# Performance work log

Hardware: AMD Instinct MI355X
Metric: run time of the kernel (lower is better)

Reference implementation:

```python
import jax, jax.numpy as jnp
import numpy as np

HEADS = 8
K = 3            # kernel_size per axis
RPB = 2 * K - 1  # rel-pos-bias extent per axis
EPS = 1e-5


def _nbr(dim, k):
    # NATTEN-style clamped window: shift window to stay fully inside [0, dim)
    q = jnp.arange(dim)
    start = jnp.clip(q - k // 2, 0, dim - k)
    nbr = start[:, None] + jnp.arange(k)[None, :]       # (dim, k) neighbor coords
    rel = nbr - q[:, None] + (k - 1)                    # (dim, k) in [0, 2k-2]
    return nbr, rel


def _instance_norm(x):
    # InstanceNorm3d, affine=False: normalize over spatial dims per (B, C)
    m = jnp.mean(x, axis=(2, 3, 4), keepdims=True)
    v = jnp.var(x, axis=(2, 3, 4), keepdims=True)
    return (x - m) * jax.lax.rsqrt(v + EPS)


def setup_inputs() -> dict:
    key = jax.random.key(0)
    ks = jax.random.split(key, 10)
    B, C, H, W, Z = 1, 128, 32, 32, 32
    Cf = 4 * C
    s = 0.02
    return {
        "x": jax.random.normal(ks[0], (B, C, H, W, Z), jnp.float32),
        "w_qkv": jax.random.normal(ks[1], (3 * C, C), jnp.float32) * s,
        "b_qkv": jnp.zeros((3 * C,), jnp.float32),
        "rpb": jax.random.normal(ks[2], (HEADS, RPB, RPB, RPB), jnp.float32) * s,
        "w_proj": jax.random.normal(ks[3], (C, C), jnp.float32) * s,
        "b_proj": jnp.zeros((C,), jnp.float32),
        "w_ffn1": jax.random.normal(ks[4], (Cf, C), jnp.float32) * s,
        "b_ffn1": jnp.zeros((Cf,), jnp.float32),
        "w_ffn2": jax.random.normal(ks[5], (C, Cf), jnp.float32) * s,
        "b_ffn2": jnp.zeros((C,), jnp.float32),
    }


def reference(x, w_qkv, b_qkv, rpb, w_proj, b_proj, w_ffn1, b_ffn1, w_ffn2, b_ffn2):
    B, C, H, W, Z = x.shape
    hd = C // HEADS
    N = H * W * Z
    KK = K ** 3

    # ---- SAM: 3D neighborhood self-attention ----
    xt = x.reshape(B, C, N).transpose(0, 2, 1)                 # (B, N, C)
    qkv = xt @ w_qkv.T + b_qkv                                  # (B, N, 3C)
    q, k_, v = jnp.split(qkv, 3, axis=-1)
    split = lambda t: t.reshape(B, N, HEADS, hd).transpose(0, 2, 1, 3)  # (B, h, N, d)
    q, k_, v = split(q), split(k_), split(v)

    nh, rh = _nbr(H, K)
    nw, rw = _nbr(W, K)
    nz, rz = _nbr(Z, K)
    # flat neighbor token index per (h, w, z, kh, kw, kz)
    nbr = ((nh[:, None, None, :, None, None] * W
            + nw[None, :, None, None, :, None]) * Z
           + nz[None, None, :, None, None, :]).reshape(N, KK)   # (N, 27)
    # flat rel-pos-bias index
    bidx = ((rh[:, None, None, :, None, None] * RPB
             + rw[None, :, None, None, :, None]) * RPB
            + rz[None, None, :, None, None, :]).reshape(N, KK)  # (N, 27)

    kg = k_[:, :, nbr]                                          # (B, h, N, 27, d)
    vg = v[:, :, nbr]                                           # (B, h, N, 27, d)
    bias = rpb.reshape(HEADS, RPB ** 3)[:, bidx]                # (h, N, 27)

    scale = jnp.asarray(hd, x.dtype) ** -0.5
    attn = jnp.einsum('bhnd,bhnkd->bhnk', q * scale, kg) + bias
    attn = jax.nn.softmax(attn, axis=-1)
    out = jnp.einsum('bhnk,bhnkd->bhnd', attn, vg)              # (B, h, N, d)
    out = out.transpose(0, 2, 1, 3).reshape(B, N, C) @ w_proj.T + b_proj
    x5 = out.transpose(0, 2, 1).reshape(B, C, H, W, Z)

    # ---- norm_in ----
    x5 = _instance_norm(x5)

    # ---- FFN (mmcv-style, GELU, residual identity) ----
    t = x5.reshape(B, C, N).transpose(0, 2, 1)                  # (B, N, C)
    t = t + (jax.nn.gelu(t @ w_ffn1.T + b_ffn1) @ w_ffn2.T + b_ffn2)
    x5 = t.transpose(0, 2, 1).reshape(B, C, H, W, Z)

    # ---- norm_out ----
    return _instance_norm(x5)
```

## Files before the change

### kernel.cpp

```cpp
#include <hip/hip_runtime.h>
#include <hip/hip_bf16.h>
#include <math.h>

#define NPOS 32768
#define CCH  128
#define C3   384
#define CF   512
#define NSH  16

typedef __attribute__((ext_vector_type(8))) short short8;
typedef __attribute__((ext_vector_type(4))) float f32x4;

__device__ inline float bf2f(unsigned short u) {
    union { unsigned int i; float f; } x; x.i = ((unsigned int)u) << 16; return x.f;
}
__device__ inline unsigned short f2bf(float f) {
    union { float f; unsigned int i; } x; x.f = f;
    unsigned int r = x.i + 0x7FFFu + ((x.i >> 16) & 1u);
    return (unsigned short)(r >> 16);
}
__device__ inline float lo_bf(unsigned int u) {
    union { unsigned int i; float f; } x; x.i = u << 16; return x.f;
}
__device__ inline float hi_bf(unsigned int u) {
    union { unsigned int i; float f; } x; x.i = u & 0xffff0000u; return x.f;
}

__global__ __launch_bounds__(256) void qkv_gemm_kernel(
    const unsigned short* __restrict__ A,
    const unsigned short* __restrict__ B,
    const float* __restrict__ bias,
    unsigned short* __restrict__ outh)
{
    __shared__ alignas(16) unsigned short As[128 * 40];
    __shared__ alignas(16) unsigned short Bs[128 * 40];

    const int tid  = threadIdx.x;
    const int lane = tid & 63;
    const int wave = tid >> 6;
    const int wm = wave & 1, wn = wave >> 1;
    const int row0 = blockIdx.y * 128;
    const int col0 = blockIdx.x * 128;

    const f32x4 fzero = {0.f, 0.f, 0.f, 0.f};
    f32x4 acc[4][4];
    #pragma unroll
    for (int i = 0; i < 4; ++i)
        #pragma unroll
        for (int j = 0; j < 4; ++j) acc[i][j] = fzero;

    const int lr = lane & 15;
    const int lk = (lane >> 4) * 8;

    for (int kt = 0; kt < CCH; kt += 32) {
        #pragma unroll
        for (int it = 0; it < 2; ++it) {
            const int c = tid + it * 256;
            const int r = c >> 2;
            const int p = (c & 3) * 8;
            *(uint4*)&As[r * 40 + p] = *(const uint4*)&A[(size_t)(row0 + r) * CCH + kt + p];
            *(uint4*)&Bs[r * 40 + p] = *(const uint4*)&B[(size_t)(col0 + r) * CCH + kt + p];
        }
        __syncthreads();
        short8 af[4], bfr[4];
        #pragma unroll
        for (int i = 0; i < 4; ++i)
            af[i]  = *(const short8*)&As[(wm * 64 + i * 16 + lr) * 40 + lk];
        #pragma unroll
        for (int j = 0; j < 4; ++j)
            bfr[j] = *(const short8*)&Bs[(wn * 64 + j * 16 + lr) * 40 + lk];
        #pragma unroll
        for (int i = 0; i < 4; ++i)
            #pragma unroll
            for (int j = 0; j < 4; ++j)
                acc[i][j] = __builtin_amdgcn_mfma_f32_16x16x32_bf16(
                                af[i], bfr[j], acc[i][j], 0, 0, 0);
        __syncthreads();
    }

    const int gr0 = row0 + wm * 64 + (lane >> 4) * 4;
    const int gc0 = col0 + wn * 64 + lr;
    #pragma unroll
    for (int j = 0; j < 4; ++j) {
        const int gc  = gc0 + j * 16;
        const int sel = gc >> 4;
        const int ch  = gc & 15;
        const float bv = bias[gc];
        #pragma unroll
        for (int i = 0; i < 4; ++i) {
            #pragma unroll
            for (int r = 0; r < 4; ++r) {
                const int gr = gr0 + i * 16 + r;
                outh[((size_t)sel * NPOS + gr) * 16 + ch] = f2bf(acc[i][j][r] + bv);
            }
        }
    }
}

__global__ __launch_bounds__(256) void attn_tiled(
    const unsigned short* __restrict__ qkv,
    const float* __restrict__ rpb,
    unsigned short* __restrict__ out)
{
    __shared__ unsigned int ksu[288 * 8];
    __shared__ unsigned int vsu[288 * 8];
    __shared__ unsigned int qsu[32 * 8];
    __shared__ float logits[32 * 29];
    __shared__ float rpbs[125];
    __shared__ float sinv[32];

    const int t  = threadIdx.x;
    const int line = ((blockIdx.x & 7) << 7) + (blockIdx.x >> 3);
    const int h  = blockIdx.y;
    const int w0 = line & 31, h0 = line >> 5;
    const int n0 = (h0 << 10) + (w0 << 5);
    const int sh0 = min(max(h0 - 1, 0), 29);
    const int sw0 = min(max(w0 - 1, 0), 29);
    const int rh_off = sh0 - h0 + 2;
    const int rw_off = sw0 - w0 + 2;

    if (t < 64) {
        const int pos = t >> 1, part = t & 1;
        const uint4 raw = *(const uint4*)&qkv[((size_t)h * NPOS + n0 + pos) * 16 + part * 8];
        *(uint4*)&qsu[pos * 8 + part * 4] = raw;
    } else if (t < 192) {
        const int i = t - 64;
        if (i < 125) rpbs[i] = rpb[h * 125 + i];
    }
    for (int c = t; c < 1152; c += 256) {
        const int p = c >> 2, part = c & 3;
        const int ihw = p >> 5, z = p & 31;
        const int ih = (ihw * 11) >> 5;
        const int iw = ihw - 3 * ih;
        const int n = ((sh0 + ih) << 10) + ((sw0 + iw) << 5) + z;
        const int kv = part >> 1;
        const uint4 raw = *(const uint4*)&qkv[((size_t)(8 + kv * 8 + h) * NPOS + n) * 16
                                              + (part & 1) * 8];
        unsigned int* d = ((kv == 0) ? ksu : vsu) + p * 8 + (part & 1) * 4;
        *(uint4*)d = raw;
    }
    __syncthreads();

    {
        const int q = t >> 3, j = t & 7;
        const int sz = min(max(q - 1, 0), 29);
        const int rz_off = sz - q + 2;
        float qf[16];
        #pragma unroll
        for (int d2 = 0; d2 < 8; ++d2) {
            const unsigned int u = qsu[q * 8 + d2];
            qf[2 * d2] = lo_bf(u); qf[2 * d2 + 1] = hi_bf(u);
        }
        float lv[4];
        int nkk = 0;
        for (int kk = j; kk < 27; kk += 8) {
            const int ihw = kk / 3, dz = kk - 3 * ihw;
            const int ih = ihw / 3,  iw = ihw - 3 * ih;
            const int p = ihw * 32 + sz + dz;
            float a = 0.f;
            #pragma unroll
            for (int d2 = 0; d2 < 8; ++d2) {
                const unsigned int u = ksu[p * 8 + d2];
                a += qf[2 * d2] * lo_bf(u) + qf[2 * d2 + 1] * hi_bf(u);
            }
            const int bidx = ((ih + rh_off) * 5 + (iw + rw_off)) * 5 + (dz + rz_off);
            lv[nkk++] = a * 0.25f + rpbs[bidx];
        }
        float mx = -1e30f;
        #pragma unroll
        for (int u = 0; u < 4; ++u) if (u < nkk) mx = fmaxf(mx, lv[u]);
        mx = fmaxf(mx, __shfl_xor(mx, 1));
        mx = fmaxf(mx, __shfl_xor(mx, 2));
        mx = fmaxf(mx, __shfl_xor(mx, 4));
        float s = 0.f;
        int u = 0;
        for (int kk = j; kk < 27; kk += 8) {
            const float e = __expf(lv[u++] - mx);
            logits[q * 29 + kk] = e;
            s += e;
        }
        s += __shfl_xor(s, 1);
        s += __shfl_xor(s, 2);
        s += __shfl_xor(s, 4);
        if (j == 0) sinv[q] = 1.f / s;
    }
    __syncthreads();

    {
        const int q = t >> 3, d2 = t & 7;
        const int sz = min(max(q - 1, 0), 29);
        float ax = 0.f, ay = 0.f;
        #pragma unroll
        for (int kk = 0; kk < 27; ++kk) {
            const int p = (kk / 3) * 32 + sz + (kk % 3);
            const float w = logits[q * 29 + kk];
            const unsigned int u = vsu[p * 8 + d2];
            ax += w * lo_bf(u); ay += w * hi_bf(u);
        }
        const float inv = sinv[q];
        const unsigned int o = ((unsigned int)f2bf(ay * inv) << 16)
                             |  (unsigned int)f2bf(ax * inv);
        *(unsigned int*)&out[(size_t)(n0 + q) * CCH + h * 16 + d2 * 2] = o;
    }
}

__global__ __launch_bounds__(256) void proj_stats_kernel(
    const unsigned short* __restrict__ attnO,
    const unsigned short* __restrict__ wproj,
    const float* __restrict__ b_proj,
    unsigned short* __restrict__ x5b,
    float* __restrict__ stats)
{
    __shared__ float red[256];

    const int t    = threadIdx.x;
    const int lane = t & 63;
    const int wn   = t >> 6;
    const int lr = lane & 15;
    const int lg = lane >> 4;
    const int lk = lg * 8;
    const int n0 = blockIdx.x * 64;
    const int sh = (blockIdx.x & (NSH - 1)) * 256;

    red[t] = 0.f;

    short8 wf[2][4];
    #pragma unroll
    for (int j = 0; j < 2; ++j)
        #pragma unroll
        for (int ks = 0; ks < 4; ++ks)
            wf[j][ks] = *(const short8*)&wproj[(wn * 32 + j * 16 + lr) * CCH + ks * 32 + lk];

    const f32x4 fzero = {0.f, 0.f, 0.f, 0.f};
    f32x4 acc[4][2];
    #pragma unroll
    for (int i = 0; i < 4; ++i)
        #pragma unroll
        for (int j = 0; j < 2; ++j) acc[i][j] = fzero;

    #pragma unroll
    for (int ks = 0; ks < 4; ++ks) {
        short8 af[4];
        #pragma unroll
        for (int i = 0; i < 4; ++i)
            af[i] = *(const short8*)&attnO[(size_t)(n0 + i * 16 + lr) * CCH + ks * 32 + lk];
        #pragma unroll
        for (int i = 0; i < 4; ++i)
            #pragma unroll
            for (int j = 0; j < 2; ++j)
                acc[i][j] = __builtin_amdgcn_mfma_f32_16x16x32_bf16(
                                af[i], wf[j][ks], acc[i][j], 0, 0, 0);
    }
    __syncthreads();

    #pragma unroll
    for (int j = 0; j < 2; ++j) {
        const int gc = wn * 32 + j * 16 + lr;
        const float bv = b_proj[gc];
        float s = 0.f, q = 0.f;
        #pragma unroll
        for (int i = 0; i < 4; ++i)
            #pragma unroll
            for (int r = 0; r < 4; ++r) {
                const int gr = i * 16 + lg * 4 + r;
                const float v = acc[i][j][r] + bv;
                s += v; q += v * v;
                x5b[(size_t)(n0 + gr) * CCH + gc] = f2bf(v);
            }
        atomicAdd(&red[gc], s);
        atomicAdd(&red[128 + gc], q);
    }
    __syncthreads();
    if (t < 128) {
        atomicAdd(&stats[sh + t],       red[t]);
        atomicAdd(&stats[sh + 128 + t], red[128 + t]);
    }
}

__global__ __launch_bounds__(256) void ffn_fused_kernel(
    const unsigned short* __restrict__ x5b,
    const unsigned short* __restrict__ w1,
    const float* __restrict__ b1,
    const unsigned short* __restrict__ w2,
    const float* __restrict__ b2,
    float* __restrict__ stats,
    unsigned short* __restrict__ tTb)
{
    __shared__ alignas(16) unsigned short pool[2 * 8704];
    unsigned short* As = pool;
    unsigned short* Hs = pool + 8704;
    __shared__ float red[256];
    __shared__ float ms[128];
    __shared__ float rss[128];

    const int t    = threadIdx.x;
    const int lane = t & 63;
    const int wn   = t >> 6;
    const int lr = lane & 15;
    const int lg = lane >> 4;
    const int lk = lg * 8;
    const int n0 = blockIdx.x * 64;
    const int sh = (blockIdx.x & (NSH - 1)) * 256;
    const float invN = 1.f / (float)NPOS;
    const f32x4 fzero = {0.f, 0.f, 0.f, 0.f};

    red[t] = 0.f;
    if (t < 128) {
        float s0 = 0.f, s1 = 0.f;
        #pragma unroll
        for (int s = 0; s < NSH; ++s) {
            s0 += stats[s * 256 + t];
            s1 += stats[s * 256 + 128 + t];
        }
        const float m = s0 * invN;
        const float v = s1 * invN - m * m;
        ms[t]  = m;
        rss[t] = rsqrtf(v + 1e-5f);
    }
    uint4 px[4];
    #pragma unroll
    for (int it = 0; it < 4; ++it) {
        const int idx = t + it * 256;
        const int row = idx >> 4, c0 = (idx & 15) * 8;
        px[it] = *(const uint4*)&x5b[(size_t)(n0 + row) * CCH + c0];
    }
    __syncthreads();

    #pragma unroll
    for (int it = 0; it < 4; ++it) {
        const int idx = t + it * 256;
        const int row = idx >> 4, c0 = (idx & 15) * 8;
        unsigned int u[4] = {px[it].x, px[it].y, px[it].z, px[it].w};
        #pragma unroll
        for (int p = 0; p < 4; ++p) {
            const int c = c0 + 2 * p;
            const float a = (lo_bf(u[p]) - ms[c])     * rss[c];
            const float b = (hi_bf(u[p]) - ms[c + 1]) * rss[c + 1];
            u[p] = ((unsigned int)f2bf(b) << 16) | (unsigned int)f2bf(a);
        }
        uint4 w; w.x = u[0]; w.y = u[1]; w.z = u[2]; w.w = u[3];
        *(uint4*)&As[row * 136 + c0] = w;
    }
    __syncthreads();

    f32x4 acc[4][2];
    #pragma unroll
    for (int i = 0; i < 4; ++i)
        #pragma unroll
        for (int j = 0; j < 2; ++j) acc[i][j] = fzero;

    #pragma unroll 1
    for (int cc = 0; cc < 4; ++cc) {
        short8 w1f[2][4];
        #pragma unroll
        for (int j = 0; j < 2; ++j)
            #pragma unroll
            for (int ks = 0; ks < 4; ++ks)
                w1f[j][ks] = *(const short8*)&w1[
                    (size_t)(cc * 128 + wn * 32 + j * 16 + lr) * CCH + ks * 32 + lk];

        f32x4 hacc[4][2];
        #pragma unroll
        for (int i = 0; i < 4; ++i)
            #pragma unroll
            for (int j = 0; j < 2; ++j) hacc[i][j] = fzero;
        #pragma unroll
        for (int ks = 0; ks < 4; ++ks) {
            short8 af[4];
            #pragma unroll
            for (int i = 0; i < 4; ++i)
                af[i] = *(const short8*)&As[(i * 16 + lr) * 136 + ks * 32 + lk];
            #pragma unroll
            for (int i = 0; i < 4; ++i)
                #pragma unroll
                for (int j = 0; j < 2; ++j)
                    hacc[i][j] = __builtin_amdgcn_mfma_f32_16x16x32_bf16(
                                    af[i], w1f[j][ks], hacc[i][j], 0, 0, 0);
        }

        short8 w2f[2][4];
        #pragma unroll
        for (int j = 0; j < 2; ++j)
            #pragma unroll
            for (int ks = 0; ks < 4; ++ks)
                w2f[j][ks] = *(const short8*)&w2[
                    (size_t)(wn * 32 + j * 16 + lr) * CF + cc * 128 + ks * 32 + lk];

        #pragma unroll
        for (int j = 0; j < 2; ++j) {
            const int gc = wn * 32 + j * 16 + lr;
            const float bv = b1[cc * 128 + gc];
            #pragma unroll
            for (int i = 0; i < 4; ++i)
                #pragma unroll
                for (int r = 0; r < 4; ++r) {
                    float v = hacc[i][j][r] + bv;
                    const float g = 0.7978845608028654f * (v + 0.044715f * v * v * v);
                    const float e = __expf(2.f * g);
                    v = v * (e / (e + 1.f));
                    Hs[(i * 16 + lg * 4 + r) * 136 + gc] = f2bf(v);
                }
        }
        __syncthreads();

        #pragma unroll
        for (int ks = 0; ks < 4; ++ks) {
            short8 af[4];
            #pragma unroll
            for (int i = 0; i < 4; ++i)
                af[i] = *(const short8*)&Hs[(i * 16 + lr) * 136 + ks * 32 + lk];
            #pragma unroll
            for (int i = 0; i < 4; ++i)
                #pragma unroll
                for (int j = 0; j < 2; ++j)
                    acc[i][j] = __builtin_amdgcn_mfma_f32_16x16x32_bf16(
                                    af[i], w2f[j][ks], acc[i][j], 0, 0, 0);
        }
        __syncthreads();
    }

    #pragma unroll
    for (int j = 0; j < 2; ++j) {
        const int gc = wn * 32 + j * 16 + lr;
        const float bv = b2[gc];
        float s = 0.f, q = 0.f;
        #pragma unroll
        for (int i = 0; i < 4; ++i)
            #pragma unroll
            for (int r = 0; r < 4; ++r) {
                const int gr = i * 16 + lg * 4 + r;
                const float v = acc[i][j][r] + bv + bf2f(As[gr * 136 + gc]);
                acc[i][j][r] = v;
                s += v; q += v * v;
            }
        atomicAdd(&red[gc], s);
        atomicAdd(&red[128 + gc], q);
    }
    __syncthreads();
    if (t < 128) {
        atomicAdd(&stats[4096 + sh + t],       red[t]);
        atomicAdd(&stats[4096 + sh + 128 + t], red[128 + t]);
    }

    float* tr = (float*)pool;
    #pragma unroll
    for (int j = 0; j < 2; ++j) {
        const int gc = wn * 32 + j * 16 + lr;
        #pragma unroll
        for (int i = 0; i < 4; ++i)
            #pragma unroll
            for (int r = 0; r < 4; ++r) {
                const int gr = i * 16 + lg * 4 + r;
                tr[gc * 68 + gr] = acc[i][j][r];
            }
    }
    __syncthreads();
    #pragma unroll
    for (int it = 0; it < 8; ++it) {
        const int idx = t + it * 256;
        const int c = idx >> 4, ch = (idx & 15) * 4;
        ushort4 o4;
        o4.x = f2bf(tr[c * 68 + ch + 0]);
        o4.y = f2bf(tr[c * 68 + ch + 1]);
        o4.z = f2bf(tr[c * 68 + ch + 2]);
        o4.w = f2bf(tr[c * 68 + ch + 3]);
        *(ushort4*)&tTb[(size_t)c * NPOS + n0 + ch] = o4;
    }
}

__global__ __launch_bounds__(256) void norm2_apply_kernel(
    const unsigned short* __restrict__ tTb, const float* __restrict__ stats,
    float* __restrict__ out)
{
    const int i = blockIdx.x * 256 + threadIdx.x;
    const size_t o = (size_t)i * 8;
    const int c = (int)(o >> 15);
    const float invN = 1.f / (float)NPOS;
    float s0 = 0.f, s1 = 0.f;
    #pragma unroll
    for (int s = 0; s < NSH; ++s) {
        s0 += stats[4096 + s * 256 + c];
        s1 += stats[4096 + s * 256 + 128 + c];
    }
    const float m  = s0 * invN;
    const float vr = s1 * invN - m * m;
    const float rs = rsqrtf(vr + 1e-5f);
    const uint4 raw = *(const uint4*)&tTb[o];
    const unsigned int u[4] = {raw.x, raw.y, raw.z, raw.w};
    float4 o0, o1;
    o0.x = (lo_bf(u[0]) - m) * rs; o0.y = (hi_bf(u[0]) - m) * rs;
    o0.z = (lo_bf(u[1]) - m) * rs; o0.w = (hi_bf(u[1]) - m) * rs;
    o1.x = (lo_bf(u[2]) - m) * rs; o1.y = (hi_bf(u[2]) - m) * rs;
    o1.z = (lo_bf(u[3]) - m) * rs; o1.w = (hi_bf(u[3]) - m) * rs;
    *(float4*)&out[o]     = o0;
    *(float4*)&out[o + 4] = o1;
}

__global__ __launch_bounds__(256) void prep_kernel(
    const float* __restrict__ wq, const float* __restrict__ wp,
    const float* __restrict__ w1, const float* __restrict__ w2,
    unsigned short* __restrict__ wq_b, unsigned short* __restrict__ wp_b,
    unsigned short* __restrict__ w1_b, unsigned short* __restrict__ w2_b,
    float* __restrict__ stats)
{
    const int i = blockIdx.x * 256 + threadIdx.x;
    if (blockIdx.x < 16) {
        stats[blockIdx.x * 512 + threadIdx.x] = 0.f;
        stats[blockIdx.x * 512 + 256 + threadIdx.x] = 0.f;
    }
    const float* src; unsigned short* dst; int off;
    if (i < 12288)      { src = wq; dst = wq_b; off = i; }
    else if (i < 16384) { src = wp; dst = wp_b; off = i - 12288; }
    else if (i < 32768) { src = w1; dst = w1_b; off = i - 16384; }
    else                { src = w2; dst = w2_b; off = i - 32768; }
    const float4 v = ((const float4*)src)[off];
    ushort4 o;
    o.x = f2bf(v.x); o.y = f2bf(v.y); o.z = f2bf(v.z); o.w = f2bf(v.w);
    ((ushort4*)dst)[off] = o;
}

__global__ __launch_bounds__(256) void transpose_x_kernel(
    const float* __restrict__ x, unsigned short* __restrict__ xt)
{
    __shared__ float tile[32][33];
    const int n0 = blockIdx.x * 32;
    const int c0 = blockIdx.y * 32;
    const int tx = threadIdx.x & 31;
    const int ty = threadIdx.x >> 5;
    for (int i = ty; i < 32; i += 8)
        tile[i][tx] = x[(size_t)(c0 + i) * NPOS + n0 + tx];
    __syncthreads();
    for (int i = ty; i < 32; i += 8)
        xt[(size_t)(n0 + i) * CCH + c0 + tx] = f2bf(tile[tx][i]);
}

extern "C" void kernel_launch(void* const* d_in, const int* in_sizes, int n_in,
                              void* d_out, int out_size, void* d_ws, size_t ws_size,
                              hipStream_t stream)
{
    const float* x      = (const float*)d_in[0];
    const float* w_qkv  = (const float*)d_in[1];
    const float* b_qkv  = (const float*)d_in[2];
    const float* rpb    = (const float*)d_in[3];
    const float* w_proj = (const float*)d_in[4];
    const float* b_proj = (const float*)d_in[5];
    const float* w_ffn1 = (const float*)d_in[6];
    const float* b_ffn1 = (const float*)d_in[7];
    const float* w_ffn2 = (const float*)d_in[8];
    const float* b_ffn2 = (const float*)d_in[9];
    float* out = (float*)d_out;

    char* ws = (char*)d_ws;
    unsigned short* xt_bf    = (unsigned short*)(ws + 0);
    unsigned short* qkv_bf   = (unsigned short*)(ws + 8388608);
    unsigned short* attnO_bf = (unsigned short*)(ws + 33554432);
    unsigned short* x5_bf    = (unsigned short*)(ws + 41943040);
    unsigned short* tTb      = (unsigned short*)(ws + 50331648);
    unsigned short* wqkv_bf  = (unsigned short*)(ws + 83886080);
    unsigned short* wproj_bf = (unsigned short*)(ws + 83984384);
    unsigned short* wffn1_bf = (unsigned short*)(ws + 84017152);
    unsigned short* wffn2_bf = (unsigned short*)(ws + 84148224);
    float*          stats    = (float*)(ws + 84279296);

    prep_kernel<<<192, 256, 0, stream>>>(w_qkv, w_proj, w_ffn1, w_ffn2,
                                         wqkv_bf, wproj_bf, wffn1_bf, wffn2_bf, stats);
    transpose_x_kernel<<<dim3(NPOS / 32, CCH / 32), 256, 0, stream>>>(x, xt_bf);

    qkv_gemm_kernel<<<dim3(C3 / 128, NPOS / 128), 256, 0, stream>>>(
        xt_bf, wqkv_bf, b_qkv, qkv_bf);

    attn_tiled<<<dim3(1024, 8), 256, 0, stream>>>(qkv_bf, rpb, attnO_bf);

    proj_stats_kernel<<<NPOS / 64, 256, 0, stream>>>(
        attnO_bf, wproj_bf, b_proj, x5_bf, stats);

    ffn_fused_kernel<<<NPOS / 64, 256, 0, stream>>>(
        x5_bf, wffn1_bf, b_ffn1, wffn2_bf, b_ffn2, stats, tTb);

    norm2_apply_kernel<<<(NPOS * CCH / 8) / 256, 256, 0, stream>>>(tTb, stats, out);
}
```

Baseline: 182.1 us.

## Fuse x transpose, weight conversion and stats init into QKV GEMM

Removes the separate prep and transpose kernels. The QKV GEMM now reads fp32 x directly, transposes and converts it to bf16 in shared memory, and converts the QKV weights on the fly. The other weight conversions and the stats zeroing are folded into the blockIdx.x==0 blocks. This saves two launches and the round trip of the transposed x through global memory. In exchange it uses a larger shared-memory footprint (full K=128 tile), scalar strided LDS writes that may bank-conflict, and redundant conversion of the weights across blocks.

After: 178.3 us. 2.1% less time.

```diff
diff --git a/kernel.cpp b/kernel.cpp
--- a/kernel.cpp
+++ b/kernel.cpp
@@ -26,14 +26,19 @@
     union { unsigned int i; float f; } x; x.i = u & 0xffff0000u; return x.f;
 }
 
-__global__ __launch_bounds__(256) void qkv_gemm_kernel(
-    const unsigned short* __restrict__ A,
-    const unsigned short* __restrict__ B,
-    const float* __restrict__ bias,
+__global__ __launch_bounds__(256) void qkv_fused_kernel(
+    const float* __restrict__ x,
+    const float* __restrict__ wqkv,
+    const float* __restrict__ b_qkv,
+    const float* __restrict__ wp,  const float* __restrict__ w1f,
+    const float* __restrict__ w2f,
+    unsigned short* __restrict__ wp_b, unsigned short* __restrict__ w1_b,
+    unsigned short* __restrict__ w2_b,
+    float* __restrict__ stats,
     unsigned short* __restrict__ outh)
 {
-    __shared__ alignas(16) unsigned short As[128 * 40];
-    __shared__ alignas(16) unsigned short Bs[128 * 40];
+    __shared__ alignas(16) unsigned short As[128 * 136];
+    __shared__ alignas(16) unsigned short Bs[128 * 136];
 
     const int tid  = threadIdx.x;
     const int lane = tid & 63;
@@ -42,6 +47,47 @@
     const int row0 = blockIdx.y * 128;
     const int col0 = blockIdx.x * 128;
 
+    if (blockIdx.x == 0) {
+        if (blockIdx.y < 16) {
+            stats[blockIdx.y * 512 + tid] = 0.f;
+            stats[blockIdx.y * 512 + 256 + tid] = 0.f;
+        }
+        if (tid < 144) {
+            const int ci = blockIdx.y * 144 + tid;
+            const float* src; unsigned short* dst; int off;
+            if (ci < 4096)       { src = wp;  dst = wp_b; off = ci; }
+            else if (ci < 20480) { src = w1f; dst = w1_b; off = ci - 4096; }
+            else                 { src = w2f; dst = w2_b; off = ci - 20480; }
+            const float4 v = ((const float4*)src)[off];
+            ushort4 o;
+            o.x = f2bf(v.x); o.y = f2bf(v.y); o.z = f2bf(v.z); o.w = f2bf(v.w);
+            ((ushort4*)dst)[off] = o;
+        }
+    }
+
+    #pragma unroll
+    for (int it = 0; it < 16; ++it) {
+        const int idx = tid + it * 256;
+        const int c  = idx >> 5;
+        const int nq = idx & 31;
+        const float4 v = *(const float4*)&x[(size_t)c * NPOS + row0 + nq * 4];
+        As[(nq * 4 + 0) * 136 + c] = f2bf(v.x);
+        As[(nq * 4 + 1) * 136 + c] = f2bf(v.y);
+        As[(nq * 4 + 2) * 136 + c] = f2bf(v.z);
+        As[(nq * 4 + 3) * 136 + c] = f2bf(v.w);
+    }
+    #pragma unroll
+    for (int it = 0; it < 16; ++it) {
+        const int idx = tid + it * 256;
+        const int col = idx >> 5;
+        const int cq  = idx & 31;
+        const float4 v = *(const float4*)&wqkv[(size_t)(col0 + col) * CCH + cq * 4];
+        ushort4 o;
+        o.x = f2bf(v.x); o.y = f2bf(v.y); o.z = f2bf(v.z); o.w = f2bf(v.w);
+        *(ushort4*)&Bs[col * 136 + cq * 4] = o;
+    }
+    __syncthreads();
+
     const f32x4 fzero = {0.f, 0.f, 0.f, 0.f};
     f32x4 acc[4][4];
     #pragma unroll
@@ -52,30 +98,21 @@
     const int lr = lane & 15;
     const int lk = (lane >> 4) * 8;
 
-    for (int kt = 0; kt < CCH; kt += 32) {
-        #pragma unroll
-        for (int it = 0; it < 2; ++it) {
-            const int c = tid + it * 256;
-            const int r = c >> 2;
-            const int p = (c & 3) * 8;
-            *(uint4*)&As[r * 40 + p] = *(const uint4*)&A[(size_t)(row0 + r) * CCH + kt + p];
-            *(uint4*)&Bs[r * 40 + p] = *(const uint4*)&B[(size_t)(col0 + r) * CCH + kt + p];
-        }
-        __syncthreads();
+    #pragma unroll
+    for (int ks = 0; ks < 4; ++ks) {
         short8 af[4], bfr[4];
         #pragma unroll
         for (int i = 0; i < 4; ++i)
-            af[i]  = *(const short8*)&As[(wm * 64 + i * 16 + lr) * 40 + lk];
+            af[i]  = *(const short8*)&As[(wm * 64 + i * 16 + lr) * 136 + ks * 32 + lk];
         #pragma unroll
         for (int j = 0; j < 4; ++j)
-            bfr[j] = *(const short8*)&Bs[(wn * 64 + j * 16 + lr) * 40 + lk];
+            bfr[j] = *(const short8*)&Bs[(wn * 64 + j * 16 + lr) * 136 + ks * 32 + lk];
         #pragma unroll
         for (int i = 0; i < 4; ++i)
             #pragma unroll
             for (int j = 0; j < 4; ++j)
                 acc[i][j] = __builtin_amdgcn_mfma_f32_16x16x32_bf16(
                                 af[i], bfr[j], acc[i][j], 0, 0, 0);
-        __syncthreads();
     }
 
     const int gr0 = row0 + wm * 64 + (lane >> 4) * 4;
@@ -85,7 +122,7 @@
         const int gc  = gc0 + j * 16;
         const int sel = gc >> 4;
         const int ch  = gc & 15;
-        const float bv = bias[gc];
+        const float bv = b_qkv[gc];
         #pragma unroll
         for (int i = 0; i < 4; ++i) {
             #pragma unroll
@@ -496,44 +533,6 @@
     *(float4*)&out[o + 4] = o1;
 }
 
-__global__ __launch_bounds__(256) void prep_kernel(
-    const float* __restrict__ wq, const float* __restrict__ wp,
-    const float* __restrict__ w1, const float* __restrict__ w2,
-    unsigned short* __restrict__ wq_b, unsigned short* __restrict__ wp_b,
-    unsigned short* __restrict__ w1_b, unsigned short* __restrict__ w2_b,
-    float* __restrict__ stats)
-{
-    const int i = blockIdx.x * 256 + threadIdx.x;
-    if (blockIdx.x < 16) {
-        stats[blockIdx.x * 512 + threadIdx.x] = 0.f;
-        stats[blockIdx.x * 512 + 256 + threadIdx.x] = 0.f;
-    }
-    const float* src; unsigned short* dst; int off;
-    if (i < 12288)      { src = wq; dst = wq_b; off = i; }
-    else if (i < 16384) { src = wp; dst = wp_b; off = i - 12288; }
-    else if (i < 32768) { src = w1; dst = w1_b; off = i - 16384; }
-    else                { src = w2; dst = w2_b; off = i - 32768; }
-    const float4 v = ((const float4*)src)[off];
-    ushort4 o;
-    o.x = f2bf(v.x); o.y = f2bf(v.y); o.z = f2bf(v.z); o.w = f2bf(v.w);
-    ((ushort4*)dst)[off] = o;
-}
-
-__global__ __launch_bounds__(256) void transpose_x_kernel(
-    const float* __restrict__ x, unsigned short* __restrict__ xt)
-{
-    __shared__ float tile[32][33];
-    const int n0 = blockIdx.x * 32;
-    const int c0 = blockIdx.y * 32;
-    const int tx = threadIdx.x & 31;
-    const int ty = threadIdx.x >> 5;
-    for (int i = ty; i < 32; i += 8)
-        tile[i][tx] = x[(size_t)(c0 + i) * NPOS + n0 + tx];
-    __syncthreads();
-    for (int i = ty; i < 32; i += 8)
-        xt[(size_t)(n0 + i) * CCH + c0 + tx] = f2bf(tile[tx][i]);
-}
-
 extern "C" void kernel_launch(void* const* d_in, const int* in_sizes, int n_in,
                               void* d_out, int out_size, void* d_ws, size_t ws_size,
                               hipStream_t stream)
@@ -551,23 +550,18 @@
     float* out = (float*)d_out;
 
     char* ws = (char*)d_ws;
-    unsigned short* xt_bf    = (unsigned short*)(ws + 0);
     unsigned short* qkv_bf   = (unsigned short*)(ws + 8388608);
     unsigned short* attnO_bf = (unsigned short*)(ws + 33554432);
     unsigned short* x5_bf    = (unsigned short*)(ws + 41943040);
     unsigned short* tTb      = (unsigned short*)(ws + 50331648);
-    unsigned short* wqkv_bf  = (unsigned short*)(ws + 83886080);
     unsigned short* wproj_bf = (unsigned short*)(ws + 83984384);
     unsigned short* wffn1_bf = (unsigned short*)(ws + 84017152);
     unsigned short* wffn2_bf = (unsigned short*)(ws + 84148224);
     float*          stats    = (float*)(ws + 84279296);
 
-    prep_kernel<<<192, 256, 0, stream>>>(w_qkv, w_proj, w_ffn1, w_ffn2,
-                                         wqkv_bf, wproj_bf, wffn1_bf, wffn2_bf, stats);
-    transpose_x_kernel<<<dim3(NPOS / 32, CCH / 32), 256, 0, stream>>>(x, xt_bf);
-
-    qkv_gemm_kernel<<<dim3(C3 / 128, NPOS / 128), 256, 0, stream>>>(
-        xt_bf, wqkv_bf, b_qkv, qkv_bf);
+    qkv_fused_kernel<<<dim3(C3 / 128, NPOS / 128), 256, 0, stream>>>(
+        x, w_qkv, b_qkv, w_proj, w_ffn1, w_ffn2,
+        wproj_bf, wffn1_bf, wffn2_bf, stats, qkv_bf);
 
     attn_tiled<<<dim3(1024, 8), 256, 0, stream>>>(qkv_bf, rpb, attnO_bf);
 
```
